# Kernel tuning notes

Measured on AMD Instinct MI355X. Metric: run time of the kernel, lower is better.

## Reference

```python
import jax, jax.numpy as jnp
import numpy as np

H, W, C, KH, KW = 16, 16, 3, 3, 3  # SOMLayer(16,16,3,3,3)
STRIDE = 2


def _extract_patches(x):
    """x: [B,C,Himg,Wimg] -> patches [B, P, C*KH*KW] in (C,kh,kw) order, P = n_out^2."""
    n_out = (x.shape[-2] - KH) // STRIDE + 1  # 15 for 32x32 input
    starts = jnp.arange(n_out) * STRIDE
    rows = starts[:, None] + jnp.arange(KH)   # [n_out, KH]
    cols = starts[:, None] + jnp.arange(KW)   # [n_out, KW]
    xr = x[:, :, rows, :]                      # [B,C,n_out,KH,Wimg]
    xrc = xr[:, :, :, :, cols]                 # [B,C,n_out,KH,n_out,KW]
    p = jnp.transpose(xrc, (0, 2, 4, 1, 3, 5)) # [B,n_out,n_out,C,KH,KW]
    return p.reshape(x.shape[0], n_out * n_out, C * KH * KW), n_out


def _som_forward(x, som):
    """Batched cdist+argmin over all windows and all 256 codebook cells.
    Faithful to the torch nested loops: winner = argmin_{m,n} mean((patch - som[m,n])^2),
    flat index m*W+n, first-occurrence tie-break (matches torch.min).
    argmin is invariant to the /27 mean scaling, so we use squared-distance GEMM form."""
    p, n_out = _extract_patches(x)             # [B,P,27]
    s = som.reshape(H * W, -1)                 # [256,27]
    d = ((p * p).sum(-1)[:, :, None]
         + (s * s).sum(-1)[None, None, :]
         - 2.0 * jnp.einsum('bpk,ck->bpc', p, s))  # [B,P,256]
    win = jnp.argmin(d, axis=-1)               # [B,P]
    m = (win // W).astype(jnp.float32) / H     # winner_r / som.shape[0]
    n = (win % W).astype(jnp.float32) / W      # winner_c / som.shape[1]
    B = x.shape[0]
    return jnp.stack([m, n], axis=1).reshape(B, 2, n_out, n_out)  # [B,2,15,15]


def setup_inputs() -> dict:
    key = jax.random.key(0)
    ks = jax.random.split(key, 10)
    B = 2048
    x = jax.random.uniform(ks[0], (B, 3, 32, 32), dtype=jnp.float32)
    # codebook (torch inits to constant 0.5 which degenerates argmin to all-ties;
    # we use a trained-like random codebook in [0,1])
    som = jax.random.uniform(ks[1], (H, W, C, KH, KW), dtype=jnp.float32)
    def lin(k, fo, fi):
        kw, kb = jax.random.split(k)
        s = 1.0 / np.sqrt(fi)
        return (jax.random.uniform(kw, (fo, fi), jnp.float32, -s, s),
                jax.random.uniform(kb, (fo,), jnp.float32, -s, s))
    W1, b1 = lin(ks[2], 400, 2 * 15 * 15)
    W2, b2 = lin(ks[3], 200, 400)
    W3, b3 = lin(ks[4], 100, 200)
    W4, b4 = lin(ks[5], 10, 100)
    return {"x": x, "som": som, "W1": W1, "b1": b1, "W2": W2, "b2": b2,
            "W3": W3, "b3": b3, "W4": W4, "b4": b4, "som_coef": 0}


def reference(x, som, W1, b1, W2, b2, W3, b3, W4, b4, som_coef):
    # som_coef=0 (and with the default momentum=1.0 the EMA update is a no-op anyway),
    # so the SOM pass is the pure winner-lookup; output is detached in torch -> stop_gradient.
    feat = jax.lax.stop_gradient(_som_forward(x, som))  # [B,2,15,15]
    h = feat.reshape(x.shape[0], -1)                    # [B,450]
    h = jax.nn.relu(h @ W1.T + b1)   # dropout in eval mode = identity
    h = jax.nn.relu(h @ W2.T + b2)
    h = jax.nn.relu(h @ W3.T + b3)
    return h @ W4.T + b4             # [B,10]
```

## Files before the change

### kernel.cpp

```cpp
#include <hip/hip_runtime.h>

#define BATCH   2048
#define NPATCH  225
#define NPTOT   (BATCH * NPATCH)
#define FKP     480
#define SOMBYTES 49152

typedef __attribute__((ext_vector_type(4))) float f32x4;
typedef __attribute__((ext_vector_type(8))) short bf16x8s;

__device__ __forceinline__ void tsplit(float v, unsigned short& h,
                                       unsigned short& m, unsigned short& l) {
    unsigned bv = __float_as_uint(v);
    h = (unsigned short)(bv >> 16);
    float r1 = v - __uint_as_float(bv & 0xFFFF0000u);
    unsigned br = __float_as_uint(r1);
    m = (unsigned short)(br >> 16);
    float r2 = r1 - __uint_as_float(br & 0xFFFF0000u);
    l = (unsigned short)(__float_as_uint(r2) >> 16);
}

__device__ __forceinline__ f32x4 mm6(bf16x8s Ah, bf16x8s Am, bf16x8s Al,
                                     bf16x8s Wh, bf16x8s Wm, bf16x8s Wl, f32x4 a) {
    a = __builtin_amdgcn_mfma_f32_16x16x32_bf16(Al, Wh, a, 0, 0, 0);
    a = __builtin_amdgcn_mfma_f32_16x16x32_bf16(Ah, Wl, a, 0, 0, 0);
    a = __builtin_amdgcn_mfma_f32_16x16x32_bf16(Am, Wm, a, 0, 0, 0);
    a = __builtin_amdgcn_mfma_f32_16x16x32_bf16(Am, Wh, a, 0, 0, 0);
    a = __builtin_amdgcn_mfma_f32_16x16x32_bf16(Ah, Wm, a, 0, 0, 0);
    a = __builtin_amdgcn_mfma_f32_16x16x32_bf16(Ah, Wh, a, 0, 0, 0);
    return a;
}

__global__ void prep_som(const float* __restrict__ som, short* __restrict__ sbuf) {
    int c = threadIdx.x;
    int ct = c >> 4, col = c & 15;
    float s2 = 0.f;
    #pragma unroll
    for (int k = 0; k < 27; ++k) { float v = som[c * 27 + k]; s2 = fmaf(v, v, s2); }
    float bias = -0.5f * s2;
    #pragma unroll
    for (int kc = 0; kc < 4; ++kc)
        #pragma unroll
        for (int j = 0; j < 8; ++j) {
            int k = kc * 8 + j;
            float v = (k < 27) ? som[c * 27 + k] : ((k == 27) ? bias : 0.f);
            unsigned short h, m, l;
            tsplit(v, h, m, l);
            int base = (ct * 192 + kc * 16 + col) * 8 + j;
            sbuf[base]        = (short)h;
            sbuf[base + 512]  = (short)m;
            sbuf[base + 1024] = (short)l;
        }
}

__global__ __launch_bounds__(256) void prep_w(
        const float* __restrict__ W1, const float* __restrict__ b1,
        const float* __restrict__ W2, const float* __restrict__ b2,
        const float* __restrict__ W3, const float* __restrict__ b3,
        const float* __restrict__ W4, const float* __restrict__ b4,
        short* __restrict__ wf1, short* __restrict__ wf2,
        short* __restrict__ wf3, short* __restrict__ wf4,
        unsigned short* __restrict__ featbf) {
    int id = blockIdx.x * 256 + threadIdx.x;
    const float* W; const float* b; short* o; int N, K, tile, ch;
    if (id < 24000) {
        tile = id >> 6; ch = id & 63; W = W1; b = b1; N = 400; K = 450;
        o = wf1 + (size_t)tile * 1536 + ch * 8;
        int kc = tile % 15, nt = tile / 15;
        int n = nt * 16 + (ch & 15), oct = ch >> 4;
        #pragma unroll
        for (int j = 0; j < 8; ++j) {
            int k = kc * 32 + oct * 8 + j;
            float v = 0.f;
            if (n < N) { if (k < K) v = W[n * K + k]; else if (k == K) v = b[n]; }
            unsigned short h, m, l; tsplit(v, h, m, l);
            o[j] = (short)h; o[512 + j] = (short)m; o[1024 + j] = (short)l;
        }
    } else if (id < 34816) {
        int id2 = id - 24000; tile = id2 >> 6; ch = id2 & 63; N = 200; K = 400;
        o = wf2 + (size_t)tile * 1536 + ch * 8;
        int kc = tile % 13, nt = tile / 13;
        int n = nt * 16 + (ch & 15), oct = ch >> 4;
        #pragma unroll
        for (int j = 0; j < 8; ++j) {
            int k = kc * 32 + oct * 8 + j;
            float v = 0.f;
            if (n < N) { if (k < K) v = W2[n * K + k]; else if (k == K) v = b2[n]; }
            unsigned short h, m, l; tsplit(v, h, m, l);
            o[j] = (short)h; o[512 + j] = (short)m; o[1024 + j] = (short)l;
        }
    } else if (id < 37952) {
        int id2 = id - 34816; tile = id2 >> 6; ch = id2 & 63; N = 100; K = 200;
        o = wf3 + (size_t)tile * 1536 + ch * 8;
        int kc = tile % 7, nt = tile / 7;
        int n = nt * 16 + (ch & 15), oct = ch >> 4;
        #pragma unroll
        for (int j = 0; j < 8; ++j) {
            int k = kc * 32 + oct * 8 + j;
            float v = 0.f;
            if (n < N) { if (k < K) v = W3[n * K + k]; else if (k == K) v = b3[n]; }
            unsigned short h, m, l; tsplit(v, h, m, l);
            o[j] = (short)h; o[512 + j] = (short)m; o[1024 + j] = (short)l;
        }
    } else if (id < 38208) {
        int id2 = id - 37952; tile = id2 >> 6; ch = id2 & 63; N = 10; K = 100;
        o = wf4 + (size_t)tile * 1536 + ch * 8;
        int kc = tile;
        int n = ch & 15, oct = ch >> 4;
        #pragma unroll
        for (int j = 0; j < 8; ++j) {
            int k = kc * 32 + oct * 8 + j;
            float v = 0.f;
            if (n < N) { if (k < K) v = W4[n * K + k]; else if (k == K) v = b4[n]; }
            unsigned short h, m, l; tsplit(v, h, m, l);
            o[j] = (short)h; o[512 + j] = (short)m; o[1024 + j] = (short)l;
        }
    } else if (id < 40256) {
        int r = id - 38208;
        unsigned short* f = featbf + (size_t)r * FKP + 450;
        f[0] = 0x3F80;
        #pragma unroll
        for (int j = 1; j < 30; ++j) f[j] = 0;
    }
}

__global__ __launch_bounds__(512, 4) void som_mfma(const float* __restrict__ x,
                                                   const short* __restrict__ sbuf,
                                                   unsigned short* __restrict__ featbf) {
    __shared__ short SB[SOMBYTES / 2];
    const int tid = threadIdx.x;
    {
        const uint4* g = (const uint4*)sbuf;
        uint4* l = (uint4*)SB;
        #pragma unroll
        for (int i = 0; i < 6; ++i) l[tid + i * 512] = g[tid + i * 512];
    }

    const int wv   = tid >> 6;
    const int lane = tid & 63;
    const int row  = lane & 15;
    const int kc   = lane >> 4;
    const int col  = lane & 15;

    bf16x8s ah[4], am[4], al[4];
    #pragma unroll
    for (int s = 0; s < 4; ++s) {
        unsigned gp = blockIdx.x * 512u + wv * 64u + s * 16u + row;
        unsigned b  = gp / 225u;
        unsigned t  = gp - b * 225u;
        unsigned oi = t / 15u, oj = t - oi * 15u;
        const float* xb = x + (size_t)b * 3072 + oi * 64 + oj * 2;
        #pragma unroll
        for (int j = 0; j < 8; ++j) {
            int k = kc * 8 + j;
            float v = 0.f;
            if (k < 27) {
                int c = k / 9, rr = k - c * 9;
                int kh = rr / 3, kw = rr - kh * 3;
                v = xb[c * 1024 + kh * 32 + kw];
            } else if (k == 27) {
                v = 1.0f;
            }
            unsigned short hh, mm, ll;
            tsplit(v, hh, mm, ll);
            ah[s][j] = (short)hh; am[s][j] = (short)mm; al[s][j] = (short)ll;
        }
    }
    __syncthreads();

    const bf16x8s* SBC = (const bf16x8s*)SB;

    f32x4 best[4];
    int   bidx[4][4];
    #pragma unroll
    for (int s = 0; s < 4; ++s) {
        best[s] = (f32x4){-1e30f, -1e30f, -1e30f, -1e30f};
        #pragma unroll
        for (int i = 0; i < 4; ++i) bidx[s][i] = 0;
    }

    #pragma unroll
    for (int ct = 0; ct < 16; ++ct) {
        bf16x8s bh = SBC[ct * 192 + lane];
        bf16x8s bm = SBC[ct * 192 + 64 + lane];
        bf16x8s bl = SBC[ct * 192 + 128 + lane];
        #pragma unroll
        for (int s = 0; s < 4; ++s) {
            f32x4 a = {0.f, 0.f, 0.f, 0.f};
            a = mm6(ah[s], am[s], al[s], bh, bm, bl, a);
            #pragma unroll
            for (int i = 0; i < 4; ++i) {
                bool g = a[i] > best[s][i];
                best[s][i] = g ? a[i] : best[s][i];
                bidx[s][i] = g ? (ct * 16 + col) : bidx[s][i];
            }
        }
    }

    #pragma unroll
    for (int m = 1; m < 16; m <<= 1) {
        #pragma unroll
        for (int s = 0; s < 4; ++s)
            #pragma unroll
            for (int i = 0; i < 4; ++i) {
                float ob = __shfl_xor(best[s][i], m, 64);
                int   oi2 = __shfl_xor(bidx[s][i], m, 64);
                if (ob > best[s][i] || (ob == best[s][i] && oi2 < bidx[s][i])) {
                    best[s][i] = ob; bidx[s][i] = oi2;
                }
            }
    }

    if (col == 0) {
        #pragma unroll
        for (int s = 0; s < 4; ++s)
            #pragma unroll
            for (int i = 0; i < 4; ++i) {
                unsigned gp2 = blockIdx.x * 512u + wv * 64u + s * 16u + kc * 4u + i;
                unsigned b2  = gp2 / 225u;
                unsigned t2  = gp2 - b2 * 225u;
                float vm = (float)(bidx[s][i] >> 4) * 0.0625f;
                float vn = (float)(bidx[s][i] & 15) * 0.0625f;
                featbf[(size_t)b2 * FKP + t2]       = (unsigned short)(__float_as_uint(vm) >> 16);
                featbf[(size_t)b2 * FKP + 225 + t2] = (unsigned short)(__float_as_uint(vn) >> 16);
            }
    }
}

#define H1S 19968
#define H2S 10752

template <int NT, int KC, int OKC, int NVALID>
__device__ __forceinline__ void layer_mid(const short* inS, short* outS,
                                          const short* __restrict__ wf,
                                          int wv, int lane) {
    const bf16x8s* Ain = (const bf16x8s*)inS;
    const int col = lane & 15, g = lane >> 4;
    constexpr int TPW = (NT + 7) / 8;
    f32x4 acc[TPW];
    #pragma unroll
    for (int i = 0; i < TPW; ++i) acc[i] = (f32x4){0.f, 0.f, 0.f, 0.f};
    #pragma unroll
    for (int kc = 0; kc < KC; ++kc) {
        bf16x8s Ah = Ain[(0 * KC + kc) * 64 + lane];
        bf16x8s Am = Ain[(1 * KC + kc) * 64 + lane];
        bf16x8s Al = Ain[(2 * KC + kc) * 64 + lane];
        #pragma unroll
        for (int ti = 0; ti < TPW; ++ti) {
            int t = wv + ti * 8;
            if (t < NT) {
                const bf16x8s* W = (const bf16x8s*)(wf + (size_t)(t * KC + kc) * 1536);
                acc[ti] = mm6(Ah, Am, Al, W[lane], W[64 + lane], W[128 + lane], acc[ti]);
            }
        }
    }
    #pragma unroll
    for (int ti = 0; ti < TPW; ++ti) {
        int t = wv + ti * 8;
        if (t < NT) {
            int k = t * 16 + col;
            if (k < NVALID) {
                int kc2 = k >> 5, oct = (k >> 3) & 3, j = k & 7;
                #pragma unroll
                for (int i = 0; i < 4; ++i) {
                    int r = g * 4 + i;
                    float v = fmaxf(acc[ti][i], 0.f);
                    unsigned short hh, mm, ll;
                    tsplit(v, hh, mm, ll);
                    outS[((0 * OKC + kc2) * 64 + oct * 16 + r) * 8 + j] = (short)hh;
                    outS[((1 * OKC + kc2) * 64 + oct * 16 + r) * 8 + j] = (short)mm;
                    outS[((2 * OKC + kc2) * 64 + oct * 16 + r) * 8 + j] = (short)ll;
                }
            }
        }
    }
}

template <int OKC, int K0, int NS>
__device__ __forceinline__ void pad_init(short* outS, int tid) {
    for (int p = tid; p < NS * 16 * 3; p += 512) {
        int term = p / (NS * 16);
        int rem  = p % (NS * 16);
        int ks   = K0 + rem / 16;
        int r    = rem % 16;
        unsigned short v = (ks == K0 && term == 0) ? 0x3F80 : 0;
        outS[((term * OKC + (ks >> 5)) * 64 + ((ks >> 3) & 3) * 16 + r) * 8 + (ks & 7)] = (short)v;
    }
}

__global__ __launch_bounds__(512) void fused_mlp(
        const unsigned short* __restrict__ featbf,
        const short* __restrict__ wf1, const short* __restrict__ wf2,
        const short* __restrict__ wf3, const short* __restrict__ wf4,
        float* __restrict__ out) {
    __shared__ short FB[H1S + H2S];

    const int tid  = threadIdx.x;
    const int wv   = tid >> 6;
    const int lane = tid & 63;
    const int col  = lane & 15, g = lane >> 4;
    const int blk  = blockIdx.x;

    const unsigned short* fb = featbf + (size_t)(blk * 16 + col) * FKP;
    bf16x8s af[15];
    #pragma unroll
    for (int kc = 0; kc < 15; ++kc)
        af[kc] = *(const bf16x8s*)(fb + kc * 32 + g * 8);

    f32x4 acc1[4];
    #pragma unroll
    for (int i = 0; i < 4; ++i) acc1[i] = (f32x4){0.f, 0.f, 0.f, 0.f};
    #pragma unroll
    for (int kc = 0; kc < 15; ++kc) {
        #pragma unroll
        for (int ti = 0; ti < 4; ++ti) {
            int t = wv + ti * 8;
            if (t < 25) {
                const bf16x8s* W = (const bf16x8s*)(wf1 + (size_t)(t * 15 + kc) * 1536);
                f32x4 a = acc1[ti];
                a = __builtin_amdgcn_mfma_f32_16x16x32_bf16(af[kc], W[128 + lane], a, 0, 0, 0);
                a = __builtin_amdgcn_mfma_f32_16x16x32_bf16(af[kc], W[64 + lane],  a, 0, 0, 0);
                a = __builtin_amdgcn_mfma_f32_16x16x32_bf16(af[kc], W[lane],       a, 0, 0, 0);
                acc1[ti] = a;
            }
        }
    }
    #pragma unroll
    for (int ti = 0; ti < 4; ++ti) {
        int t = wv + ti * 8;
        if (t < 25) {
            int k = t * 16 + col;
            int kc2 = k >> 5, oct = (k >> 3) & 3, j = k & 7;
            #pragma unroll
            for (int i = 0; i < 4; ++i) {
                int r = g * 4 + i;
                float v = fmaxf(acc1[ti][i], 0.f);
                unsigned short hh, mm, ll;
                tsplit(v, hh, mm, ll);
                FB[((0 * 13 + kc2) * 64 + oct * 16 + r) * 8 + j] = (short)hh;
                FB[((1 * 13 + kc2) * 64 + oct * 16 + r) * 8 + j] = (short)mm;
                FB[((2 * 13 + kc2) * 64 + oct * 16 + r) * 8 + j] = (short)ll;
            }
        }
    }
    pad_init<13, 400, 16>(FB, tid);
    __syncthreads();

    layer_mid<13, 13, 7, 200>(FB, FB + H1S, wf2, wv, lane);
    pad_init<7, 200, 24>(FB + H1S, tid);
    __syncthreads();

    layer_mid<7, 7, 4, 100>(FB + H1S, FB, wf3, wv, lane);
    pad_init<4, 100, 28>(FB, tid);
    __syncthreads();

    if (wv == 0) {
        const bf16x8s* Ain = (const bf16x8s*)FB;
        f32x4 a = {0.f, 0.f, 0.f, 0.f};
        #pragma unroll
        for (int kc = 0; kc < 4; ++kc) {
            bf16x8s Ah = Ain[(0 * 4 + kc) * 64 + lane];
            bf16x8s Am = Ain[(1 * 4 + kc) * 64 + lane];
            bf16x8s Al = Ain[(2 * 4 + kc) * 64 + lane];
            const bf16x8s* W = (const bf16x8s*)(wf4 + (size_t)kc * 1536);
            a = mm6(Ah, Am, Al, W[lane], W[64 + lane], W[128 + lane], a);
        }
        if (col < 10) {
            #pragma unroll
            for (int i = 0; i < 4; ++i)
                out[(size_t)(blk * 16 + g * 4 + i) * 10 + col] = a[i];
        }
    }
}

extern "C" void kernel_launch(void* const* d_in, const int* in_sizes, int n_in,
                              void* d_out, int out_size, void* d_ws, size_t ws_size,
                              hipStream_t stream) {
    const float* x   = (const float*)d_in[0];
    const float* som = (const float*)d_in[1];
    const float* W1  = (const float*)d_in[2];
    const float* b1  = (const float*)d_in[3];
    const float* W2  = (const float*)d_in[4];
    const float* b2  = (const float*)d_in[5];
    const float* W3  = (const float*)d_in[6];
    const float* b3  = (const float*)d_in[7];
    const float* W4  = (const float*)d_in[8];
    const float* b4  = (const float*)d_in[9];

    char* ws = (char*)d_ws;
    short*          sbuf   = (short*)ws;
    unsigned short* featbf = (unsigned short*)(ws + 49152);
    short*          wf1    = (short*)(ws + 2015232);
    short*          wf2    = (short*)(ws + 3167232);
    short*          wf3    = (short*)(ws + 3686400);
    short*          wf4    = (short*)(ws + 3836928);
    float* outp = (float*)d_out;

    prep_som<<<1, 256, 0, stream>>>(som, sbuf);
    prep_w<<<158, 256, 0, stream>>>(W1, b1, W2, b2, W3, b3, W4, b4,
                                    wf1, wf2, wf3, wf4, featbf);
    som_mfma<<<900, 512, 0, stream>>>(x, sbuf, featbf);
    fused_mlp<<<128, 512, 0, stream>>>(featbf, wf1, wf2, wf3, wf4, outp);
}
```

Before: 195.3 us.

## Merge prep kernels and software-pipeline weight loads in fused MLP with split accumulators

Folds the codebook preparation into the weight-prep kernel, saving one launch. In the fused MLP, weight fragments for the next k-chunk and tile are prefetched into registers before the current MFMAs are issued. The six-MFMA split-precision chain is also split across two independent accumulators to shorten the dependency chain. Together these aim to hide global-load latency and MFMA back-to-back stalls, at the cost of more registers, which the new launch bound of 2 blocks per CU constrains.

```diff
diff --git a/kernel.cpp b/kernel.cpp
--- a/kernel.cpp
+++ b/kernel.cpp
@@ -8,6 +8,8 @@
 
 typedef __attribute__((ext_vector_type(4))) float f32x4;
 typedef __attribute__((ext_vector_type(8))) short bf16x8s;
+
+#define MFMA(A,B,C) __builtin_amdgcn_mfma_f32_16x16x32_bf16(A, B, C, 0, 0, 0)
 
 __device__ __forceinline__ void tsplit(float v, unsigned short& h,
                                        unsigned short& m, unsigned short& l) {
@@ -22,96 +24,71 @@
 
 __device__ __forceinline__ f32x4 mm6(bf16x8s Ah, bf16x8s Am, bf16x8s Al,
                                      bf16x8s Wh, bf16x8s Wm, bf16x8s Wl, f32x4 a) {
-    a = __builtin_amdgcn_mfma_f32_16x16x32_bf16(Al, Wh, a, 0, 0, 0);
-    a = __builtin_amdgcn_mfma_f32_16x16x32_bf16(Ah, Wl, a, 0, 0, 0);
-    a = __builtin_amdgcn_mfma_f32_16x16x32_bf16(Am, Wm, a, 0, 0, 0);
-    a = __builtin_amdgcn_mfma_f32_16x16x32_bf16(Am, Wh, a, 0, 0, 0);
-    a = __builtin_amdgcn_mfma_f32_16x16x32_bf16(Ah, Wm, a, 0, 0, 0);
-    a = __builtin_amdgcn_mfma_f32_16x16x32_bf16(Ah, Wh, a, 0, 0, 0);
+    a = MFMA(Al, Wh, a); a = MFMA(Ah, Wl, a); a = MFMA(Am, Wm, a);
+    a = MFMA(Am, Wh, a); a = MFMA(Ah, Wm, a); a = MFMA(Ah, Wh, a);
     return a;
 }
 
-__global__ void prep_som(const float* __restrict__ som, short* __restrict__ sbuf) {
-    int c = threadIdx.x;
-    int ct = c >> 4, col = c & 15;
-    float s2 = 0.f;
-    #pragma unroll
-    for (int k = 0; k < 27; ++k) { float v = som[c * 27 + k]; s2 = fmaf(v, v, s2); }
-    float bias = -0.5f * s2;
-    #pragma unroll
-    for (int kc = 0; kc < 4; ++kc)
-        #pragma unroll
-        for (int j = 0; j < 8; ++j) {
-            int k = kc * 8 + j;
-            float v = (k < 27) ? som[c * 27 + k] : ((k == 27) ? bias : 0.f);
-            unsigned short h, m, l;
-            tsplit(v, h, m, l);
-            int base = (ct * 192 + kc * 16 + col) * 8 + j;
-            sbuf[base]        = (short)h;
-            sbuf[base + 512]  = (short)m;
-            sbuf[base + 1024] = (short)l;
-        }
-}
-
-__global__ __launch_bounds__(256) void prep_w(
+__global__ __launch_bounds__(256) void prep_all(
+        const float* __restrict__ som,
         const float* __restrict__ W1, const float* __restrict__ b1,
         const float* __restrict__ W2, const float* __restrict__ b2,
         const float* __restrict__ W3, const float* __restrict__ b3,
         const float* __restrict__ W4, const float* __restrict__ b4,
+        short* __restrict__ sbuf,
         short* __restrict__ wf1, short* __restrict__ wf2,
         short* __restrict__ wf3, short* __restrict__ wf4,
         unsigned short* __restrict__ featbf) {
     int id = blockIdx.x * 256 + threadIdx.x;
-    const float* W; const float* b; short* o; int N, K, tile, ch;
     if (id < 24000) {
-        tile = id >> 6; ch = id & 63; W = W1; b = b1; N = 400; K = 450;
-        o = wf1 + (size_t)tile * 1536 + ch * 8;
+        int tile = id >> 6, ch = id & 63;
+        short* o = wf1 + (size_t)tile * 1536 + ch * 8;
         int kc = tile % 15, nt = tile / 15;
         int n = nt * 16 + (ch & 15), oct = ch >> 4;
         #pragma unroll
         for (int j = 0; j < 8; ++j) {
             int k = kc * 32 + oct * 8 + j;
             float v = 0.f;
-            if (n < N) { if (k < K) v = W[n * K + k]; else if (k == K) v = b[n]; }
+            if (n < 400) { if (k < 450) v = W1[n * 450 + k]; else if (k == 450) v = b1[n]; }
             unsigned short h, m, l; tsplit(v, h, m, l);
             o[j] = (short)h; o[512 + j] = (short)m; o[1024 + j] = (short)l;
         }
     } else if (id < 34816) {
-        int id2 = id - 24000; tile = id2 >> 6; ch = id2 & 63; N = 200; K = 400;
-        o = wf2 + (size_t)tile * 1536 + ch * 8;
+        int id2 = id - 24000, tile = id2 >> 6, ch = id2 & 63;
+        short* o = wf2 + (size_t)tile * 1536 + ch * 8;
         int kc = tile % 13, nt = tile / 13;
         int n = nt * 16 + (ch & 15), oct = ch >> 4;
         #pragma unroll
         for (int j = 0; j < 8; ++j) {
             int k = kc * 32 + oct * 8 + j;
             float v = 0.f;
-            if (n < N) { if (k < K) v = W2[n * K + k]; else if (k == K) v = b2[n]; }
+            if (n < 200) { if (k < 400) v = W2[n * 400 + k]; else if (k == 400) v = b2[n]; }
             unsigned short h, m, l; tsplit(v, h, m, l);
             o[j] = (short)h; o[512 + j] = (short)m; o[1024 + j] = (short)l;
         }
     } else if (id < 37952) {
-        int id2 = id - 34816; tile = id2 >> 6; ch = id2 & 63; N = 100; K = 200;
-        o = wf3 + (size_t)tile * 1536 + ch * 8;
+        int id2 = id - 34816, tile = id2 >> 6, ch = id2 & 63;
+        short* o = wf3 + (size_t)tile * 1536 + ch * 8;
         int kc = tile % 7, nt = tile / 7;
         int n = nt * 16 + (ch & 15), oct = ch >> 4;
         #pragma unroll
         for (int j = 0; j < 8; ++j) {
             int k = kc * 32 + oct * 8 + j;
             float v = 0.f;
-            if (n < N) { if (k < K) v = W3[n * K + k]; else if (k == K) v = b3[n]; }
+            if (n < 100) { if (k < 200) v = W3[n * 200 + k]; else if (k == 200) v = b3[n]; }
             unsigned short h, m, l; tsplit(v, h, m, l);
             o[j] = (short)h; o[512 + j] = (short)m; o[1024 + j] = (short)l;
         }
     } else if (id < 38208) {
-        int id2 = id - 37952; tile = id2 >> 6; ch = id2 & 63; N = 10; K = 100;
-        o = wf4 + (size_t)tile * 1536 + ch * 8;
+        int id2 = id - 37952, tile = id2 >> 6, ch = id2 & 63;
+        short* o = wf4 + (size_t)tile * 1536 + ch * 8;
         int kc = tile;
         int n = ch & 15, oct = ch >> 4;
         #pragma unroll
         for (int j = 0; j < 8; ++j) {
             int k = kc * 32 + oct * 8 + j;
             float v = 0.f;
-            if (n < N) { if (k < K) v = W4[n * K + k]; else if (k == K) v = b4[n]; }
+            if (n < 10) { if (k < 100) v = W4[n * 100 + k]; else if (k == 100) v = b4[n]; }
             unsigned short h, m, l; tsplit(v, h, m, l);
             o[j] = (short)h; o[512 + j] = (short)m; o[1024 + j] = (short)l;
         }
@@ -121,6 +98,26 @@
         f[0] = 0x3F80;
         #pragma unroll
         for (int j = 1; j < 30; ++j) f[j] = 0;
+    } else if (id < 40512) {
+        int c = id - 40256;
+        int ct = c >> 4, col = c & 15;
+        float s2 = 0.f;
+        #pragma unroll
+        for (int k = 0; k < 27; ++k) { float v = som[c * 27 + k]; s2 = fmaf(v, v, s2); }
+        float bias = -0.5f * s2;
+        #pragma unroll
+        for (int kc = 0; kc < 4; ++kc)
+            #pragma unroll
+            for (int j = 0; j < 8; ++j) {
+                int k = kc * 8 + j;
+                float v = (k < 27) ? som[c * 27 + k] : ((k == 27) ? bias : 0.f);
+                unsigned short h, m, l;
+                tsplit(v, h, m, l);
+                int base = (ct * 192 + kc * 16 + col) * 8 + j;
+                sbuf[base]        = (short)h;
+                sbuf[base + 512]  = (short)m;
+                sbuf[base + 1024] = (short)l;
+            }
     }
 }
 
@@ -231,46 +228,89 @@
 #define H2S 10752
 
 template <int NT, int KC, int OKC, int NVALID>
-__device__ __forceinline__ void layer_mid(const short* inS, short* outS,
-                                          const short* __restrict__ wf,
-                                          int wv, int lane) {
+__device__ __forceinline__ void layer_mid2(const short* inS, short* outS,
+                                           const short* __restrict__ wf,
+                                           int wv, int lane) {
     const bf16x8s* Ain = (const bf16x8s*)inS;
+    const bf16x8s* Wb  = (const bf16x8s*)wf;
     const int col = lane & 15, g = lane >> 4;
-    constexpr int TPW = (NT + 7) / 8;
-    f32x4 acc[TPW];
-    #pragma unroll
-    for (int i = 0; i < TPW; ++i) acc[i] = (f32x4){0.f, 0.f, 0.f, 0.f};
+    const bool v0 = (wv < NT);
+    const int t0 = v0 ? wv : 0;
+    constexpr bool TWO = (NT > 8);
+    const bool v1 = TWO && (wv + 8 < NT);
+    const int t1 = v1 ? (wv + 8) : (NT - 1);
+
+    f32x4 a0A = {0.f,0.f,0.f,0.f}, a0B = {0.f,0.f,0.f,0.f};
+    f32x4 a1A = {0.f,0.f,0.f,0.f}, a1B = {0.f,0.f,0.f,0.f};
+
+    bf16x8s Ah = Ain[(0 * KC) * 64 + lane];
+    bf16x8s Am = Ain[(1 * KC) * 64 + lane];
+    bf16x8s Al = Ain[(2 * KC) * 64 + lane];
+    bf16x8s w0h = Wb[(size_t)(t0 * KC) * 192 + lane];
+    bf16x8s w0m = Wb[(size_t)(t0 * KC) * 192 + 64 + lane];
+    bf16x8s w0l = Wb[(size_t)(t0 * KC) * 192 + 128 + lane];
+    bf16x8s w1h, w1m, w1l;
+    if constexpr (TWO) {
+        w1h = Wb[(size_t)(t1 * KC) * 192 + lane];
+        w1m = Wb[(size_t)(t1 * KC) * 192 + 64 + lane];
+        w1l = Wb[(size_t)(t1 * KC) * 192 + 128 + lane];
+    }
+
     #pragma unroll
     for (int kc = 0; kc < KC; ++kc) {
-        bf16x8s Ah = Ain[(0 * KC + kc) * 64 + lane];
-        bf16x8s Am = Ain[(1 * KC + kc) * 64 + lane];
-        bf16x8s Al = Ain[(2 * KC + kc) * 64 + lane];
-        #pragma unroll
-        for (int ti = 0; ti < TPW; ++ti) {
-            int t = wv + ti * 8;
-            if (t < NT) {
-                const bf16x8s* W = (const bf16x8s*)(wf + (size_t)(t * KC + kc) * 1536);
-                acc[ti] = mm6(Ah, Am, Al, W[lane], W[64 + lane], W[128 + lane], acc[ti]);
-            }
-        }
-    }
-    #pragma unroll
-    for (int ti = 0; ti < TPW; ++ti) {
-        int t = wv + ti * 8;
-        if (t < NT) {
-            int k = t * 16 + col;
-            if (k < NVALID) {
-                int kc2 = k >> 5, oct = (k >> 3) & 3, j = k & 7;
-                #pragma unroll
-                for (int i = 0; i < 4; ++i) {
-                    int r = g * 4 + i;
-                    float v = fmaxf(acc[ti][i], 0.f);
-                    unsigned short hh, mm, ll;
-                    tsplit(v, hh, mm, ll);
-                    outS[((0 * OKC + kc2) * 64 + oct * 16 + r) * 8 + j] = (short)hh;
-                    outS[((1 * OKC + kc2) * 64 + oct * 16 + r) * 8 + j] = (short)mm;
-                    outS[((2 * OKC + kc2) * 64 + oct * 16 + r) * 8 + j] = (short)ll;
-                }
+        const int kn = (kc + 1 < KC) ? kc + 1 : kc;
+        bf16x8s nAh = Ain[(0 * KC + kn) * 64 + lane];
+        bf16x8s nAm = Ain[(1 * KC + kn) * 64 + lane];
+        bf16x8s nAl = Ain[(2 * KC + kn) * 64 + lane];
+        bf16x8s n0h = Wb[(size_t)(t0 * KC + kn) * 192 + lane];
+        bf16x8s n0m = Wb[(size_t)(t0 * KC + kn) * 192 + 64 + lane];
+        bf16x8s n0l = Wb[(size_t)(t0 * KC + kn) * 192 + 128 + lane];
+        bf16x8s n1h, n1m, n1l;
+        if constexpr (TWO) {
+            n1h = Wb[(size_t)(t1 * KC + kn) * 192 + lane];
+            n1m = Wb[(size_t)(t1 * KC + kn) * 192 + 64 + lane];
+            n1l = Wb[(size_t)(t1 * KC + kn) * 192 + 128 + lane];
+        }
+        a0A = MFMA(Al, w0h, a0A);  if constexpr (TWO) a1A = MFMA(Al, w1h, a1A);
+        a0B = MFMA(Ah, w0l, a0B);  if constexpr (TWO) a1B = MFMA(Ah, w1l, a1B);
+        a0A = MFMA(Am, w0m, a0A);  if constexpr (TWO) a1A = MFMA(Am, w1m, a1A);
+        a0B = MFMA(Am, w0h, a0B);  if constexpr (TWO) a1B = MFMA(Am, w1h, a1B);
+        a0A = MFMA(Ah, w0m, a0A);  if constexpr (TWO) a1A = MFMA(Ah, w1m, a1A);
+        a0B = MFMA(Ah, w0h, a0B);  if constexpr (TWO) a1B = MFMA(Ah, w1h, a1B);
+        Ah = nAh; Am = nAm; Al = nAl;
+        w0h = n0h; w0m = n0m; w0l = n0l;
+        if constexpr (TWO) { w1h = n1h; w1m = n1m; w1l = n1l; }
+    }
+
+    {
+        int kk = wv * 16 + col;
+        if (v0 && kk < NVALID) {
+            int kc2 = kk >> 5, oct = (kk >> 3) & 3, j = kk & 7;
+            #pragma unroll
+            for (int i = 0; i < 4; ++i) {
+                int r = g * 4 + i;
+                float vv = fmaxf(a0A[i] + a0B[i], 0.f);
+                unsigned short hh, mm, ll;
+                tsplit(vv, hh, mm, ll);
+                outS[((0 * OKC + kc2) * 64 + oct * 16 + r) * 8 + j] = (short)hh;
+                outS[((1 * OKC + kc2) * 64 + oct * 16 + r) * 8 + j] = (short)mm;
+                outS[((2 * OKC + kc2) * 64 + oct * 16 + r) * 8 + j] = (short)ll;
+            }
+        }
+    }
+    if constexpr (TWO) {
+        int kk = (wv + 8) * 16 + col;
+        if (v1 && kk < NVALID) {
+            int kc2 = kk >> 5, oct = (kk >> 3) & 3, j = kk & 7;
+            #pragma unroll
+            for (int i = 0; i < 4; ++i) {
+                int r = g * 4 + i;
+                float vv = fmaxf(a1A[i] + a1B[i], 0.f);
+                unsigned short hh, mm, ll;
+                tsplit(vv, hh, mm, ll);
+                outS[((0 * OKC + kc2) * 64 + oct * 16 + r) * 8 + j] = (short)hh;
+                outS[((1 * OKC + kc2) * 64 + oct * 16 + r) * 8 + j] = (short)mm;
+                outS[((2 * OKC + kc2) * 64 + oct * 16 + r) * 8 + j] = (short)ll;
             }
         }
     }
@@ -288,7 +328,7 @@
     }
 }
 
-__global__ __launch_bounds__(512) void fused_mlp(
+__global__ __launch_bounds__(512, 2) void fused_mlp(
         const unsigned short* __restrict__ featbf,
         const short* __restrict__ wf1, const short* __restrict__ wf2,
         const short* __restrict__ wf3, const short* __restrict__ wf4,
@@ -310,19 +350,29 @@
     f32x4 acc1[4];
     #pragma unroll
     for (int i = 0; i < 4; ++i) acc1[i] = (f32x4){0.f, 0.f, 0.f, 0.f};
-    #pragma unroll
-    for (int kc = 0; kc < 15; ++kc) {
-        #pragma unroll
-        for (int ti = 0; ti < 4; ++ti) {
-            int t = wv + ti * 8;
+
+    {
+        const bf16x8s* Wb = (const bf16x8s*)wf1;
+        int tl0 = wv;
+        bf16x8s cl = Wb[(size_t)(tl0 * 15) * 192 + 128 + lane];
+        bf16x8s cm = Wb[(size_t)(tl0 * 15) * 192 + 64 + lane];
+        bf16x8s ch = Wb[(size_t)(tl0 * 15) * 192 + lane];
+        #pragma unroll
+        for (int u = 0; u < 60; ++u) {
+            const int kc = u >> 2, tu = u & 3;
+            const int t  = wv + tu * 8;
+            const int un = (u + 1 < 60) ? u + 1 : u;
+            const int knc = un >> 2;
+            int tn = wv + (un & 3) * 8; if (tn > 24) tn = 24;
+            bf16x8s nl = Wb[(size_t)(tn * 15 + knc) * 192 + 128 + lane];
+            bf16x8s nm = Wb[(size_t)(tn * 15 + knc) * 192 + 64 + lane];
+            bf16x8s nh = Wb[(size_t)(tn * 15 + knc) * 192 + lane];
             if (t < 25) {
-                const bf16x8s* W = (const bf16x8s*)(wf1 + (size_t)(t * 15 + kc) * 1536);
-                f32x4 a = acc1[ti];
-                a = __builtin_amdgcn_mfma_f32_16x16x32_bf16(af[kc], W[128 + lane], a, 0, 0, 0);
-                a = __builtin_amdgcn_mfma_f32_16x16x32_bf16(af[kc], W[64 + lane],  a, 0, 0, 0);
-                a = __builtin_amdgcn_mfma_f32_16x16x32_bf16(af[kc], W[lane],       a, 0, 0, 0);
-                acc1[ti] = a;
-            }
+                acc1[tu] = MFMA(af[kc], cl, acc1[tu]);
+                acc1[tu] = MFMA(af[kc], cm, acc1[tu]);
+                acc1[tu] = MFMA(af[kc], ch, acc1[tu]);
+            }
+            cl = nl; cm = nm; ch = nh;
         }
     }
     #pragma unroll
@@ -346,29 +396,32 @@
     pad_init<13, 400, 16>(FB, tid);
     __syncthreads();
 
-    layer_mid<13, 13, 7, 200>(FB, FB + H1S, wf2, wv, lane);
+    layer_mid2<13, 13, 7, 200>(FB, FB + H1S, wf2, wv, lane);
     pad_init<7, 200, 24>(FB + H1S, tid);
     __syncthreads();
 
-    layer_mid<7, 7, 4, 100>(FB + H1S, FB, wf3, wv, lane);
+    layer_mid2<7, 7, 4, 100>(FB + H1S, FB, wf3, wv, lane);
     pad_init<4, 100, 28>(FB, tid);
     __syncthreads();
 
     if (wv == 0) {
         const bf16x8s* Ain = (const bf16x8s*)FB;
-        f32x4 a = {0.f, 0.f, 0.f, 0.f};
+        f32x4 aA = {0.f, 0.f, 0.f, 0.f}, aB = {0.f, 0.f, 0.f, 0.f};
         #pragma unroll
         for (int kc = 0; kc < 4; ++kc) {
             bf16x8s Ah = Ain[(0 * 4 + kc) * 64 + lane];
             bf16x8s Am = Ain[(1 * 4 + kc) * 64 + lane];
             bf16x8s Al = Ain[(2 * 4 + kc) * 64 + lane];
             const bf16x8s* W = (const bf16x8s*)(wf4 + (size_t)kc * 1536);
-            a = mm6(Ah, Am, Al, W[lane], W[64 + lane], W[128 + lane], a);
+            bf16x8s wh = W[lane], wm = W[64 + lane], wl = W[128 + lane];
+            aA = MFMA(Al, wh, aA);  aB = MFMA(Ah, wl, aB);
+            aA = MFMA(Am, wm, aA);  aB = MFMA(Am, wh, aB);
+            aA = MFMA(Ah, wm, aA);  aB = MFMA(Ah, wh, aB);
         }
         if (col < 10) {
             #pragma unroll
             for (int i = 0; i < 4; ++i)
-                out[(size_t)(blk * 16 + g * 4 + i) * 10 + col] = a[i];
+                out[(size_t)(blk * 16 + g * 4 + i) * 10 + col] = aA[i] + aB[i];
         }
     }
 }
@@ -396,9 +449,8 @@
     short*          wf4    = (short*)(ws + 3836928);
     float* outp = (float*)d_out;
 
-    prep_som<<<1, 256, 0, stream>>>(som, sbuf);
-    prep_w<<<158, 256, 0, stream>>>(W1, b1, W2, b2, W3, b3, W4, b4,
-                                    wf1, wf2, wf3, wf4, featbf);
+    prep_all<<<159, 256, 0, stream>>>(som, W1, b1, W2, b2, W3, b3, W4, b4,
+                                      sbuf, wf1, wf2, wf3, wf4, featbf);
     som_mfma<<<900, 512, 0, stream>>>(x, sbuf, featbf);
     fused_mlp<<<128, 512, 0, stream>>>(featbf, wf1, wf2, wf3, wf4, outp);
 }
```

New measurement: 177.0 us. -9.3%, faster.
